# Performance work log

Measured on AMD Instinct MI355X. Metric: run time of the kernel, lower is better.

Reference implementation:

```python
import jax, jax.numpy as jnp
import numpy as np

D_MODEL, D_K, D_V, H, B = 1024, 64, 64, 16, 32768


def _xavier(key, fan_in, fan_out):
    std = float(np.sqrt(2.0 / (fan_in + fan_out)))
    return jax.random.normal(key, (fan_in, fan_out), dtype=jnp.float32) * std


def setup_inputs() -> dict:
    key = jax.random.key(0)
    ks = jax.random.split(key, 7)
    return {
        "queries": jax.random.normal(ks[0], (B, D_MODEL), dtype=jnp.float32),
        "keys": jax.random.normal(ks[1], (B, D_MODEL), dtype=jnp.float32),
        "values": jax.random.normal(ks[2], (B, D_MODEL), dtype=jnp.float32),
        "Wq": _xavier(ks[3], D_MODEL, H * D_K),
        "bq": jnp.zeros((H * D_K,), jnp.float32),
        "Wk": _xavier(ks[4], D_MODEL, H * D_K),
        "bk": jnp.zeros((H * D_K,), jnp.float32),
        "Wv": _xavier(ks[5], D_MODEL, H * D_V),
        "bv": jnp.zeros((H * D_V,), jnp.float32),
        "Wo": _xavier(ks[6], H * D_V, D_MODEL),
        "bo": jnp.zeros((D_MODEL,), jnp.float32),
    }


def reference(queries, keys, values, Wq, bq, Wk, bk, Wv, bv, Wo, bo):
    b = queries.shape[0]
    q = (queries @ Wq + bq).reshape(b, H, D_K)   # (b, h, d_k)
    k = (keys @ Wk + bk).reshape(b, H, D_K)      # (b, h, d_k)
    v = (values @ Wv + bv).reshape(b, H, D_V)    # (b, h, d_v)
    # attention over heads: (b, h, h)
    att = jnp.einsum('bhd,bgd->bhg', q, k) / jnp.sqrt(jnp.float32(D_K))
    att = jax.nn.softmax(att, axis=-1)
    out = jnp.einsum('bhg,bgd->bhd', att, v).reshape(b, H * D_V)
    return out @ Wo + bo
```

## Files before the change

kernel.cpp:

```cpp
#include <hip/hip_runtime.h>

typedef __attribute__((ext_vector_type(8))) unsigned short u16x8;
typedef __attribute__((ext_vector_type(8))) short s16x8;
typedef __attribute__((ext_vector_type(4))) float f32x4;

#define D_MODEL 1024
#define NROWS 32768
#define BK 64
#define NT 16

__device__ __forceinline__ unsigned short f2bf(float f) {
  union { float f; unsigned int u; } c; c.f = f;
  return (unsigned short)((c.u + 0x7fffu + ((c.u >> 16) & 1u)) >> 16);
}
__device__ __forceinline__ float bf2f(unsigned short h) {
  union { unsigned int u; float f; } c; c.u = ((unsigned int)h) << 16;
  return c.f;
}

__device__ __forceinline__ void gload_lds16(const void* gsrc, void* ldst) {
  const __attribute__((address_space(1))) void* g =
      reinterpret_cast<const __attribute__((address_space(1))) void*>(
          reinterpret_cast<unsigned long long>(gsrc));
  __attribute__((address_space(3))) void* l =
      reinterpret_cast<__attribute__((address_space(3))) void*>(
          static_cast<unsigned int>(reinterpret_cast<unsigned long long>(ldst)));
  __builtin_amdgcn_global_load_lds(g, l, 16, 0, 0);
}

#define BAR() asm volatile("s_barrier" ::: "memory")

__global__ __launch_bounds__(256) void wtrans_kernel(
    const float* __restrict__ W0, const float* __restrict__ W1,
    const float* __restrict__ W2, const float* __restrict__ W3,
    unsigned short* __restrict__ T0, unsigned short* __restrict__ T1,
    unsigned short* __restrict__ T2, unsigned short* __restrict__ T3) {
  const float* W = blockIdx.z == 0 ? W0 : blockIdx.z == 1 ? W1 : blockIdx.z == 2 ? W2 : W3;
  unsigned short* T = blockIdx.z == 0 ? T0 : blockIdx.z == 1 ? T1 : blockIdx.z == 2 ? T2 : T3;
  __shared__ float tile[32][33];
  const int tx = threadIdx.x & 31, ty = threadIdx.x >> 5;
  const int n0 = blockIdx.x * 32, k0 = blockIdx.y * 32;
#pragma unroll
  for (int i = 0; i < 4; ++i)
    tile[ty + 8 * i][tx] = W[(size_t)(k0 + ty + 8 * i) * D_MODEL + n0 + tx];
  __syncthreads();
#pragma unroll
  for (int i = 0; i < 4; ++i)
    T[(size_t)(n0 + ty + 8 * i) * D_MODEL + k0 + tx] = f2bf(tile[tx][ty + 8 * i]);
}

__global__ __launch_bounds__(256) void xconvert(
    const float* __restrict__ X0, const float* __restrict__ X1, const float* __restrict__ X2,
    unsigned short* __restrict__ Y0, unsigned short* __restrict__ Y1,
    unsigned short* __restrict__ Y2) {
  const float* X = blockIdx.z == 0 ? X0 : blockIdx.z == 1 ? X1 : X2;
  unsigned short* Y = blockIdx.z == 0 ? Y0 : blockIdx.z == 1 ? Y1 : Y2;
  const int NCH = (NROWS * D_MODEL) / 8;
  for (int c = blockIdx.x * 256 + threadIdx.x; c < NCH; c += gridDim.x * 256) {
    f32x4 f0 = *(const f32x4*)(X + (size_t)c * 8);
    f32x4 f1 = *(const f32x4*)(X + (size_t)c * 8 + 4);
    u16x8 h;
#pragma unroll
    for (int e = 0; e < 4; ++e) { h[e] = f2bf(f0[e]); h[4 + e] = f2bf(f1[e]); }
    *(u16x8*)(Y + (size_t)c * 8) = h;
  }
}

#define MFMA16(p, A00, A01, A10, A11)                                                        \
  _Pragma("unroll") for (int n = 0; n < 4; ++n) {                                            \
    acc[2*(p)][n]   = __builtin_amdgcn_mfma_f32_16x16x32_bf16(A00, bfr[n][0], acc[2*(p)][n], 0, 0, 0);   \
    acc[2*(p)][n]   = __builtin_amdgcn_mfma_f32_16x16x32_bf16(A01, bfr[n][1], acc[2*(p)][n], 0, 0, 0);   \
    acc[2*(p)+1][n] = __builtin_amdgcn_mfma_f32_16x16x32_bf16(A10, bfr[n][0], acc[2*(p)+1][n], 0, 0, 0); \
    acc[2*(p)+1][n] = __builtin_amdgcn_mfma_f32_16x16x32_bf16(A11, bfr[n][1], acc[2*(p)+1][n], 0, 0, 0); \
  }

#define LDA_(Ac, m, ksoff) (*(const s16x8*)((Ac) + (wm * 128 + (m) * 16 + lrow) * 128 + (ksoff)))
#define LDB_(Bc, n, ksoff) (*(const s16x8*)((Bc) + (wn * 64 + (n) * 16 + lrow) * 128 + (ksoff)))

template <bool OUT_BF16>
__device__ __forceinline__ void gemm8p_body(
    const unsigned short* __restrict__ A, const unsigned short* __restrict__ BT,
    const float* __restrict__ bias, void* __restrict__ Cp, char* smem) {
  const int tid = threadIdx.x;
  const int lane = tid & 63, wid = tid >> 6;
  const int wm = wid >> 2, wn = wid & 3;
  const int lrow = lane & 15, lkg = lane >> 4;

  const int id = blockIdx.y * gridDim.x + blockIdx.x;
  const int sw = (id & 7) * 64 + (id >> 3);
  const int mbase = (sw >> 2) * 256;
  const int nbase = (sw & 3) * 256;

  char* const Ab0 = smem;
  char* const Ab1 = smem + 32768;
  char* const Bb0 = smem + 65536;
  char* const Bb1 = smem + 98304;

  const int sgoff = (((tid & 7) ^ ((tid >> 3) & 7)) * 8);
  const int srow = tid >> 3;
  const int soff0 = ((0 + lkg) ^ (lrow & 7)) * 16;
  const int soff1 = ((4 + lkg) ^ (lrow & 7)) * 16;
  const int ldsw = wid * 1024;

  auto stA = [&](int u, int half) {
    const unsigned short* G =
        A + (size_t)(mbase + half * 128 + srow) * D_MODEL + u * BK + sgoff;
    char* L = ((u & 1) ? Ab1 : Ab0) + half * 16384 + ldsw;
    gload_lds16(G, L);
    gload_lds16(G + (size_t)64 * D_MODEL, L + 8192);
  };
  auto stB = [&](int u, int half) {
    const unsigned short* G =
        BT + (size_t)(nbase + half * 128 + srow) * D_MODEL + u * BK + sgoff;
    char* L = ((u & 1) ? Bb1 : Bb0) + half * 16384 + ldsw;
    gload_lds16(G, L);
    gload_lds16(G + (size_t)64 * D_MODEL, L + 8192);
  };

  f32x4 acc[8][4];
  f32x4 zero = {0.f, 0.f, 0.f, 0.f};
#pragma unroll
  for (int m = 0; m < 8; ++m)
#pragma unroll
    for (int n = 0; n < 4; ++n) acc[m][n] = zero;
  s16x8 bfr[4][2];

  stA(0, 0); stA(0, 1); stB(0, 0); stB(0, 1);
  stB(1, 0); stB(1, 1);
  asm volatile("s_waitcnt vmcnt(4)" ::: "memory");
  BAR();

#pragma unroll 1
  for (int u = 0; u < NT; ++u) {
    char* Ac = (u & 1) ? Ab1 : Ab0;
    char* Bc = (u & 1) ? Bb1 : Bb0;
    {
      s16x8 a00 = LDA_(Ac, 0, soff0), a01 = LDA_(Ac, 0, soff1);
      s16x8 a10 = LDA_(Ac, 1, soff0), a11 = LDA_(Ac, 1, soff1);
#pragma unroll
      for (int n = 0; n < 4; ++n) { bfr[n][0] = LDB_(Bc, n, soff0); bfr[n][1] = LDB_(Bc, n, soff1); }
      if (u + 1 < NT) stA(u + 1, 0);
      BAR();
      __builtin_amdgcn_s_setprio(1);
      MFMA16(0, a00, a01, a10, a11);
      __builtin_amdgcn_s_setprio(0);
      BAR();
    }
    {
      s16x8 a00 = LDA_(Ac, 2, soff0), a01 = LDA_(Ac, 2, soff1);
      s16x8 a10 = LDA_(Ac, 3, soff0), a11 = LDA_(Ac, 3, soff1);
      if (u + 1 < NT) stA(u + 1, 1);
      BAR();
      __builtin_amdgcn_s_setprio(1);
      MFMA16(1, a00, a01, a10, a11);
      __builtin_amdgcn_s_setprio(0);
      BAR();
    }
    {
      s16x8 a00 = LDA_(Ac, 4, soff0), a01 = LDA_(Ac, 4, soff1);
      s16x8 a10 = LDA_(Ac, 5, soff0), a11 = LDA_(Ac, 5, soff1);
      if (u + 2 < NT) stB(u + 2, 0);
      BAR();
      __builtin_amdgcn_s_setprio(1);
      MFMA16(2, a00, a01, a10, a11);
      __builtin_amdgcn_s_setprio(0);
      BAR();
    }
    {
      s16x8 a00 = LDA_(Ac, 6, soff0), a01 = LDA_(Ac, 6, soff1);
      s16x8 a10 = LDA_(Ac, 7, soff0), a11 = LDA_(Ac, 7, soff1);
      if (u + 2 < NT) {
        stB(u + 2, 1);
        asm volatile("s_waitcnt vmcnt(4)" ::: "memory");
      } else {
        asm volatile("s_waitcnt vmcnt(0)" ::: "memory");
      }
      BAR();
      __builtin_amdgcn_s_setprio(1);
      MFMA16(3, a00, a01, a10, a11);
      __builtin_amdgcn_s_setprio(0);
      BAR();
    }
  }

  const size_t crow0 = mbase + wm * 128;
  const int ccol0 = nbase + wn * 64;
#pragma unroll
  for (int m = 0; m < 8; ++m) {
#pragma unroll
    for (int n = 0; n < 4; ++n) {
      const int col = ccol0 + n * 16 + lrow;
      const float bv = bias[col];
#pragma unroll
      for (int r = 0; r < 4; ++r) {
        const size_t row = crow0 + m * 16 + lkg * 4 + r;
        const float v = acc[m][n][r] + bv;
        if constexpr (OUT_BF16)
          ((unsigned short*)Cp)[row * D_MODEL + col] = f2bf(v);
        else
          ((float*)Cp)[row * D_MODEL + col] = v;
      }
    }
  }
}

__global__ __launch_bounds__(512, 1) void qkv_gemm8(
    const unsigned short* __restrict__ Xq, const unsigned short* __restrict__ Xk,
    const unsigned short* __restrict__ Xv,
    const unsigned short* __restrict__ WqT, const unsigned short* __restrict__ WkT,
    const unsigned short* __restrict__ WvT,
    const float* __restrict__ bq, const float* __restrict__ bk, const float* __restrict__ bv,
    unsigned short* __restrict__ Qb, unsigned short* __restrict__ Kb,
    unsigned short* __restrict__ Vb) {
  extern __shared__ char smem[];
  const int z = blockIdx.z;
  gemm8p_body<true>(z == 0 ? Xq : z == 1 ? Xk : Xv,
                    z == 0 ? WqT : z == 1 ? WkT : WvT,
                    z == 0 ? bq : z == 1 ? bk : bv,
                    z == 0 ? (void*)Qb : z == 1 ? (void*)Kb : (void*)Vb, smem);
}

__global__ __launch_bounds__(512, 1) void out_gemm8(
    const unsigned short* __restrict__ Ob, const unsigned short* __restrict__ WoT,
    const float* __restrict__ bo, float* __restrict__ out) {
  extern __shared__ char smem[];
  gemm8p_body<false>(Ob, WoT, bo, out, smem);
}

__global__ __launch_bounds__(256) void attn_kernel(
    const unsigned short* __restrict__ Qb, const unsigned short* __restrict__ Kb,
    const unsigned short* __restrict__ Vb, unsigned short* __restrict__ Ob) {
  __shared__ __align__(16) unsigned short sm[4][3][16 * 72];
  const int tid = threadIdx.x, lane = tid & 63, wid = tid >> 6;
  const size_t row = (size_t)blockIdx.x * 4 + wid;
  const unsigned short* srcs[3] = {Qb + row * 1024, Kb + row * 1024, Vb + row * 1024};
#pragma unroll
  for (int m = 0; m < 3; ++m) {
#pragma unroll
    for (int i = 0; i < 2; ++i) {
      int c = lane * 2 + i;
      int h = c >> 3, col = (c & 7) * 8;
      *(u16x8*)&sm[wid][m][h * 72 + col] = *(const u16x8*)(srcs[m] + h * 64 + col);
    }
  }
  __syncthreads();

  const int h = lane & 15, gq = lane >> 4;
  float s[4] = {0.f, 0.f, 0.f, 0.f};
#pragma unroll
  for (int dc = 0; dc < 8; ++dc) {
    u16x8 qv = *(const u16x8*)&sm[wid][0][h * 72 + dc * 8];
    float qf[8];
#pragma unroll
    for (int e = 0; e < 8; ++e) qf[e] = bf2f(qv[e]);
#pragma unroll
    for (int j = 0; j < 4; ++j) {
      u16x8 kv = *(const u16x8*)&sm[wid][1][(gq * 4 + j) * 72 + dc * 8];
#pragma unroll
      for (int e = 0; e < 8; ++e) s[j] += qf[e] * bf2f(kv[e]);
    }
  }
  float mx = s[0];
#pragma unroll
  for (int j = 0; j < 4; ++j) { s[j] *= 0.125f; mx = fmaxf(mx * (j == 0 ? 0.125f : 1.f), s[j]); }
  mx = fmaxf(mx, __shfl_xor(mx, 16, 64));
  mx = fmaxf(mx, __shfl_xor(mx, 32, 64));
  float p[4], sum = 0.f;
#pragma unroll
  for (int j = 0; j < 4; ++j) { p[j] = __expf(s[j] - mx); sum += p[j]; }
  sum += __shfl_xor(sum, 16, 64);
  sum += __shfl_xor(sum, 32, 64);
  const float rinv = 1.0f / sum;
  float pall[16];
#pragma unroll
  for (int t = 0; t < 4; ++t)
#pragma unroll
    for (int j = 0; j < 4; ++j) pall[t * 4 + j] = __shfl(p[j], h + 16 * t, 64);
  float o[16];
#pragma unroll
  for (int e = 0; e < 16; ++e) o[e] = 0.f;
  const int db = gq * 16;
#pragma unroll
  for (int g = 0; g < 16; ++g) {
    float pg = pall[g];
    u16x8 v0 = *(const u16x8*)&sm[wid][2][g * 72 + db];
    u16x8 v1 = *(const u16x8*)&sm[wid][2][g * 72 + db + 8];
#pragma unroll
    for (int e = 0; e < 8; ++e) { o[e] += pg * bf2f(v0[e]); o[8 + e] += pg * bf2f(v1[e]); }
  }
  u16x8 r0, r1;
#pragma unroll
  for (int e = 0; e < 8; ++e) { r0[e] = f2bf(o[e] * rinv); r1[e] = f2bf(o[8 + e] * rinv); }
  unsigned short* dst = Ob + row * 1024 + h * 64 + db;
  *(u16x8*)dst = r0;
  *(u16x8*)(dst + 8) = r1;
}

extern "C" void kernel_launch(void* const* d_in, const int* in_sizes, int n_in,
                              void* d_out, int out_size, void* d_ws, size_t ws_size,
                              hipStream_t stream) {
  const float* queries = (const float*)d_in[0];
  const float* keys    = (const float*)d_in[1];
  const float* values  = (const float*)d_in[2];
  const float* Wq = (const float*)d_in[3];
  const float* bq = (const float*)d_in[4];
  const float* Wk = (const float*)d_in[5];
  const float* bk = (const float*)d_in[6];
  const float* Wv = (const float*)d_in[7];
  const float* bv = (const float*)d_in[8];
  const float* Wo = (const float*)d_in[9];
  const float* bo = (const float*)d_in[10];
  float* out = (float*)d_out;

  unsigned short* ws = (unsigned short*)d_ws;
  const size_t WE = (size_t)1024 * 1024;
  const size_t XE = (size_t)NROWS * 1024;
  unsigned short* WqT = ws;
  unsigned short* WkT = WqT + WE;
  unsigned short* WvT = WkT + WE;
  unsigned short* WoT = WvT + WE;
  unsigned short* Xcq = WoT + WE;
  unsigned short* Xck = Xcq + XE;
  unsigned short* Xcv = Xck + XE;
  unsigned short* Qb  = Xcv + XE;
  unsigned short* Kb  = Qb + XE;
  unsigned short* Vb  = Kb + XE;
  unsigned short* Ob  = Xcq;

  hipFuncSetAttribute((const void*)qkv_gemm8, hipFuncAttributeMaxDynamicSharedMemorySize, 131072);
  hipFuncSetAttribute((const void*)out_gemm8, hipFuncAttributeMaxDynamicSharedMemorySize, 131072);

  wtrans_kernel<<<dim3(32, 32, 4), 256, 0, stream>>>(Wq, Wk, Wv, Wo, WqT, WkT, WvT, WoT);
  xconvert<<<dim3(2048, 1, 3), 256, 0, stream>>>(queries, keys, values, Xcq, Xck, Xcv);
  qkv_gemm8<<<dim3(4, 128, 3), 512, 131072, stream>>>(
      Xcq, Xck, Xcv, WqT, WkT, WvT, bq, bk, bv, Qb, Kb, Vb);
  attn_kernel<<<dim3(NROWS / 4), 256, 0, stream>>>(Qb, Kb, Vb, Ob);
  out_gemm8<<<dim3(4, 128, 1), 512, 131072, stream>>>(Ob, WoT, bo, out);
}
```

Measured before the change: 486.2 us.

## Fuse fp32-to-bf16 input conversion into QKV GEMM A-tile loading

Removes the separate conversion kernel that turned the three fp32 input matrices into bf16 copies. The QKV GEMM now loads fp32 A tiles into registers, packs them with v_cvt_pk_bf16_f32 and writes them swizzled into LDS. This avoids writing and re-reading the bf16 intermediates. In exchange, the GEMM reads twice the bytes for A, loses the async global-to-LDS path for A, and adds full vmcnt/lgkmcnt waits inside the main loop.

```diff
diff --git a/kernel.cpp b/kernel.cpp
--- a/kernel.cpp
+++ b/kernel.cpp
@@ -16,6 +16,11 @@
 __device__ __forceinline__ float bf2f(unsigned short h) {
   union { unsigned int u; float f; } c; c.u = ((unsigned int)h) << 16;
   return c.f;
+}
+__device__ __forceinline__ unsigned int cvtpk_bf16(float lo, float hi) {
+  unsigned int r;
+  asm("v_cvt_pk_bf16_f32 %0, %1, %2" : "=v"(r) : "v"(lo), "v"(hi));
+  return r;
 }
 
 __device__ __forceinline__ void gload_lds16(const void* gsrc, void* ldst) {
@@ -49,23 +54,6 @@
     T[(size_t)(n0 + ty + 8 * i) * D_MODEL + k0 + tx] = f2bf(tile[tx][ty + 8 * i]);
 }
 
-__global__ __launch_bounds__(256) void xconvert(
-    const float* __restrict__ X0, const float* __restrict__ X1, const float* __restrict__ X2,
-    unsigned short* __restrict__ Y0, unsigned short* __restrict__ Y1,
-    unsigned short* __restrict__ Y2) {
-  const float* X = blockIdx.z == 0 ? X0 : blockIdx.z == 1 ? X1 : X2;
-  unsigned short* Y = blockIdx.z == 0 ? Y0 : blockIdx.z == 1 ? Y1 : Y2;
-  const int NCH = (NROWS * D_MODEL) / 8;
-  for (int c = blockIdx.x * 256 + threadIdx.x; c < NCH; c += gridDim.x * 256) {
-    f32x4 f0 = *(const f32x4*)(X + (size_t)c * 8);
-    f32x4 f1 = *(const f32x4*)(X + (size_t)c * 8 + 4);
-    u16x8 h;
-#pragma unroll
-    for (int e = 0; e < 4; ++e) { h[e] = f2bf(f0[e]); h[4 + e] = f2bf(f1[e]); }
-    *(u16x8*)(Y + (size_t)c * 8) = h;
-  }
-}
-
 #define MFMA16(p, A00, A01, A10, A11)                                                        \
   _Pragma("unroll") for (int n = 0; n < 4; ++n) {                                            \
     acc[2*(p)][n]   = __builtin_amdgcn_mfma_f32_16x16x32_bf16(A00, bfr[n][0], acc[2*(p)][n], 0, 0, 0);   \
@@ -77,9 +65,9 @@
 #define LDA_(Ac, m, ksoff) (*(const s16x8*)((Ac) + (wm * 128 + (m) * 16 + lrow) * 128 + (ksoff)))
 #define LDB_(Bc, n, ksoff) (*(const s16x8*)((Bc) + (wn * 64 + (n) * 16 + lrow) * 128 + (ksoff)))
 
-template <bool OUT_BF16>
+template <bool A_FP32, bool OUT_BF16>
 __device__ __forceinline__ void gemm8p_body(
-    const unsigned short* __restrict__ A, const unsigned short* __restrict__ BT,
+    const void* __restrict__ Ap, const unsigned short* __restrict__ BT,
     const float* __restrict__ bias, void* __restrict__ Cp, char* smem) {
   const int tid = threadIdx.x;
   const int lane = tid & 63, wid = tid >> 6;
@@ -104,7 +92,7 @@
 
   auto stA = [&](int u, int half) {
     const unsigned short* G =
-        A + (size_t)(mbase + half * 128 + srow) * D_MODEL + u * BK + sgoff;
+        (const unsigned short*)Ap + (size_t)(mbase + half * 128 + srow) * D_MODEL + u * BK + sgoff;
     char* L = ((u & 1) ? Ab1 : Ab0) + half * 16384 + ldsw;
     gload_lds16(G, L);
     gload_lds16(G + (size_t)64 * D_MODEL, L + 8192);
@@ -117,6 +105,35 @@
     gload_lds16(G + (size_t)64 * D_MODEL, L + 8192);
   };
 
+  f32x4 fa[8];
+  auto ldA = [&](int u, int half) {
+    const float* G = (const float*)Ap +
+        (size_t)(mbase + half * 128 + srow) * D_MODEL + u * BK + (tid & 7) * 8;
+    fa[half * 4 + 0] = *(const f32x4*)G;
+    fa[half * 4 + 1] = *(const f32x4*)(G + 4);
+    fa[half * 4 + 2] = *(const f32x4*)(G + (size_t)64 * D_MODEL);
+    fa[half * 4 + 3] = *(const f32x4*)(G + (size_t)64 * D_MODEL + 4);
+  };
+  auto wrA = [&](int u) {
+    char* Abuf = ((u & 1) ? Ab1 : Ab0);
+#pragma unroll
+    for (int h = 0; h < 2; ++h) {
+#pragma unroll
+      for (int rr = 0; rr < 2; ++rr) {
+        f32x4 lo = fa[h * 4 + rr * 2 + 0];
+        f32x4 hi = fa[h * 4 + rr * 2 + 1];
+        union { unsigned int w[4]; u16x8 v; } pk;
+        pk.w[0] = cvtpk_bf16(lo[0], lo[1]);
+        pk.w[1] = cvtpk_bf16(lo[2], lo[3]);
+        pk.w[2] = cvtpk_bf16(hi[0], hi[1]);
+        pk.w[3] = cvtpk_bf16(hi[2], hi[3]);
+        const int r = srow + rr * 64;
+        *(u16x8*)(Abuf + h * 16384 + r * 128 + (((tid & 7) ^ (r & 7)) * 16)) = pk.v;
+      }
+    }
+    asm volatile("s_waitcnt lgkmcnt(0)" ::: "memory");
+  };
+
   f32x4 acc[8][4];
   f32x4 zero = {0.f, 0.f, 0.f, 0.f};
 #pragma unroll
@@ -125,9 +142,18 @@
     for (int n = 0; n < 4; ++n) acc[m][n] = zero;
   s16x8 bfr[4][2];
 
-  stA(0, 0); stA(0, 1); stB(0, 0); stB(0, 1);
-  stB(1, 0); stB(1, 1);
-  asm volatile("s_waitcnt vmcnt(4)" ::: "memory");
+  if constexpr (A_FP32) {
+    ldA(0, 0); ldA(0, 1);
+    stB(0, 0); stB(0, 1);
+    stB(1, 0); stB(1, 1);
+    asm volatile("s_waitcnt vmcnt(8)" ::: "memory");
+    wrA(0);
+    asm volatile("s_waitcnt vmcnt(4)" ::: "memory");
+  } else {
+    stA(0, 0); stA(0, 1); stB(0, 0); stB(0, 1);
+    stB(1, 0); stB(1, 1);
+    asm volatile("s_waitcnt vmcnt(4)" ::: "memory");
+  }
   BAR();
 
 #pragma unroll 1
@@ -139,7 +165,7 @@
       s16x8 a10 = LDA_(Ac, 1, soff0), a11 = LDA_(Ac, 1, soff1);
 #pragma unroll
       for (int n = 0; n < 4; ++n) { bfr[n][0] = LDB_(Bc, n, soff0); bfr[n][1] = LDB_(Bc, n, soff1); }
-      if (u + 1 < NT) stA(u + 1, 0);
+      if (u + 1 < NT) { if constexpr (A_FP32) ldA(u + 1, 0); else stA(u + 1, 0); }
       BAR();
       __builtin_amdgcn_s_setprio(1);
       MFMA16(0, a00, a01, a10, a11);
@@ -149,7 +175,7 @@
     {
       s16x8 a00 = LDA_(Ac, 2, soff0), a01 = LDA_(Ac, 2, soff1);
       s16x8 a10 = LDA_(Ac, 3, soff0), a11 = LDA_(Ac, 3, soff1);
-      if (u + 1 < NT) stA(u + 1, 1);
+      if (u + 1 < NT) { if constexpr (A_FP32) ldA(u + 1, 1); else stA(u + 1, 1); }
       BAR();
       __builtin_amdgcn_s_setprio(1);
       MFMA16(1, a00, a01, a10, a11);
@@ -159,6 +185,10 @@
     {
       s16x8 a00 = LDA_(Ac, 4, soff0), a01 = LDA_(Ac, 4, soff1);
       s16x8 a10 = LDA_(Ac, 5, soff0), a11 = LDA_(Ac, 5, soff1);
+      if constexpr (A_FP32) {
+        asm volatile("s_waitcnt vmcnt(0)" ::: "memory");
+        if (u + 1 < NT) wrA(u + 1);
+      }
       if (u + 2 < NT) stB(u + 2, 0);
       BAR();
       __builtin_amdgcn_s_setprio(1);
@@ -169,11 +199,13 @@
     {
       s16x8 a00 = LDA_(Ac, 6, soff0), a01 = LDA_(Ac, 6, soff1);
       s16x8 a10 = LDA_(Ac, 7, soff0), a11 = LDA_(Ac, 7, soff1);
-      if (u + 2 < NT) {
-        stB(u + 2, 1);
-        asm volatile("s_waitcnt vmcnt(4)" ::: "memory");
-      } else {
-        asm volatile("s_waitcnt vmcnt(0)" ::: "memory");
+      if (u + 2 < NT) stB(u + 2, 1);
+      if constexpr (!A_FP32) {
+        if (u + 2 < NT) {
+          asm volatile("s_waitcnt vmcnt(4)" ::: "memory");
+        } else {
+          asm volatile("s_waitcnt vmcnt(0)" ::: "memory");
+        }
       }
       BAR();
       __builtin_amdgcn_s_setprio(1);
@@ -205,8 +237,7 @@
 }
 
 __global__ __launch_bounds__(512, 1) void qkv_gemm8(
-    const unsigned short* __restrict__ Xq, const unsigned short* __restrict__ Xk,
-    const unsigned short* __restrict__ Xv,
+    const float* __restrict__ Xq, const float* __restrict__ Xk, const float* __restrict__ Xv,
     const unsigned short* __restrict__ WqT, const unsigned short* __restrict__ WkT,
     const unsigned short* __restrict__ WvT,
     const float* __restrict__ bq, const float* __restrict__ bk, const float* __restrict__ bv,
@@ -214,17 +245,17 @@
     unsigned short* __restrict__ Vb) {
   extern __shared__ char smem[];
   const int z = blockIdx.z;
-  gemm8p_body<true>(z == 0 ? Xq : z == 1 ? Xk : Xv,
-                    z == 0 ? WqT : z == 1 ? WkT : WvT,
-                    z == 0 ? bq : z == 1 ? bk : bv,
-                    z == 0 ? (void*)Qb : z == 1 ? (void*)Kb : (void*)Vb, smem);
+  gemm8p_body<true, true>(z == 0 ? (const void*)Xq : z == 1 ? (const void*)Xk : (const void*)Xv,
+                          z == 0 ? WqT : z == 1 ? WkT : WvT,
+                          z == 0 ? bq : z == 1 ? bk : bv,
+                          z == 0 ? (void*)Qb : z == 1 ? (void*)Kb : (void*)Vb, smem);
 }
 
 __global__ __launch_bounds__(512, 1) void out_gemm8(
     const unsigned short* __restrict__ Ob, const unsigned short* __restrict__ WoT,
     const float* __restrict__ bo, float* __restrict__ out) {
   extern __shared__ char smem[];
-  gemm8p_body<false>(Ob, WoT, bo, out, smem);
+  gemm8p_body<false, false>(Ob, WoT, bo, out, smem);
 }
 
 __global__ __launch_bounds__(256) void attn_kernel(
@@ -319,21 +350,17 @@
   unsigned short* WkT = WqT + WE;
   unsigned short* WvT = WkT + WE;
   unsigned short* WoT = WvT + WE;
-  unsigned short* Xcq = WoT + WE;
-  unsigned short* Xck = Xcq + XE;
-  unsigned short* Xcv = Xck + XE;
-  unsigned short* Qb  = Xcv + XE;
+  unsigned short* Qb  = WoT + WE;
   unsigned short* Kb  = Qb + XE;
   unsigned short* Vb  = Kb + XE;
-  unsigned short* Ob  = Xcq;
+  unsigned short* Ob  = Vb + XE;
 
   hipFuncSetAttribute((const void*)qkv_gemm8, hipFuncAttributeMaxDynamicSharedMemorySize, 131072);
   hipFuncSetAttribute((const void*)out_gemm8, hipFuncAttributeMaxDynamicSharedMemorySize, 131072);
 
   wtrans_kernel<<<dim3(32, 32, 4), 256, 0, stream>>>(Wq, Wk, Wv, Wo, WqT, WkT, WvT, WoT);
-  xconvert<<<dim3(2048, 1, 3), 256, 0, stream>>>(queries, keys, values, Xcq, Xck, Xcv);
   qkv_gemm8<<<dim3(4, 128, 3), 512, 131072, stream>>>(
-      Xcq, Xck, Xcv, WqT, WkT, WvT, bq, bk, bv, Qb, Kb, Vb);
+      queries, keys, values, WqT, WkT, WvT, bq, bk, bv, Qb, Kb, Vb);
   attn_kernel<<<dim3(NROWS / 4), 256, 0, stream>>>(Qb, Kb, Vb, Ob);
   out_gemm8<<<dim3(4, 128, 1), 512, 131072, stream>>>(Ob, WoT, bo, out);
 }
```

Result: faster. 445.1 us (-8.4%).
